# Kernel optimization log

Measured on AMD Instinct MI355X. Metric: run time of the kernel, lower is better.

The kernel has to match this reference:

```python
import jax, jax.numpy as jnp
import numpy as np

N_NODES = 100000
IN_DIM = 256
OUT_DIM = 128
N_EDGES = 3200000


def setup_inputs() -> dict:
    key = jax.random.key(0)
    k1, k2, k3, k4, k5, k6 = jax.random.split(key, 6)
    stdv = 1.0 / np.sqrt(OUT_DIM)
    return {
        "feature_map": jax.random.normal(k1, (N_NODES, IN_DIM), dtype=jnp.float32),
        "edge_src": jax.random.randint(k2, (N_EDGES,), 0, N_NODES, dtype=jnp.int32),
        "edge_dst": jax.random.randint(k3, (N_EDGES,), 0, N_NODES, dtype=jnp.int32),
        "edge_vals": jax.random.uniform(k4, (N_EDGES,), dtype=jnp.float32),
        "weights": jax.random.uniform(k5, (IN_DIM, OUT_DIM), dtype=jnp.float32, minval=-stdv, maxval=stdv),
        "b": jax.random.uniform(k6, (OUT_DIM,), dtype=jnp.float32, minval=-stdv, maxval=stdv),
    }


def reference(feature_map, edge_src, edge_dst, edge_vals, weights, b):
    # dense feature transform: [N, in] @ [in, out] -> [N, out]
    h = feature_map @ weights
    # sparse adjacency matmul A @ h via edge list:
    # out[dst] += A[dst, src] * h[src]
    msgs = edge_vals[:, None] * h[edge_src]  # [E, out]
    out = jax.ops.segment_sum(msgs, edge_dst, num_segments=N_NODES)
    # fused bias add epilogue
    return out + b
```

## Files before the change

### kernel.cpp

```cpp
#include <hip/hip_runtime.h>

#define N_NODES 100000
#define IN_DIM 256
#define OUT_DIM 128
#define N_EDGES 3200000

#define NB 3125
#define CAP 1280
#define PTILE 6400
#define PBLK 500
#define GBLK 782

typedef __attribute__((ext_vector_type(8))) short short8;
typedef __attribute__((ext_vector_type(4))) float float4v;

__device__ __forceinline__ unsigned short f2bf(float f) {
    union { float f; unsigned int u; } v; v.f = f;
    unsigned int r = v.u + 0x7FFF + ((v.u >> 16) & 1);
    return (unsigned short)(r >> 16);
}

__global__ __launch_bounds__(256) void setup_kernel(const float* __restrict__ W,
                                                    unsigned short* __restrict__ Wf,
                                                    int* __restrict__ cursor) {
    if (blockIdx.x < 16) {
        const int f = blockIdx.x * 256 + threadIdx.x;
        const int lane = f & 63;
        const int qc = f >> 6;
        const int q = qc >> 3, ct = qc & 7;
        const int n = ct * 16 + (lane & 15);
        const int k0 = q * 32 + (lane >> 4) * 8;
        unsigned int o[4];
#pragma unroll
        for (int jj = 0; jj < 4; ++jj) {
            const unsigned short lo = f2bf(W[(k0 + 2 * jj) * OUT_DIM + n]);
            const unsigned short hi = f2bf(W[(k0 + 2 * jj + 1) * OUT_DIM + n]);
            o[jj] = (unsigned)lo | ((unsigned)hi << 16);
        }
        ((uint4*)Wf)[f] = make_uint4(o[0], o[1], o[2], o[3]);
    } else {
        const int i = (blockIdx.x - 16) * 256 + threadIdx.x;
        if (i < NB) cursor[i] = 0;
    }
}

__global__ __launch_bounds__(512, 4) void fused_kernel(const float* __restrict__ X,
                                                       const unsigned short* __restrict__ Wf,
                                                       unsigned short* __restrict__ hb,
                                                       const int* __restrict__ src,
                                                       const int* __restrict__ dst,
                                                       const float* __restrict__ vals,
                                                       int* __restrict__ cursor,
                                                       int2* __restrict__ pairs) {
    __shared__ int smem[8192];
    const int tid = threadIdx.x;
    const int bx = blockIdx.x;
    const bool is_part = (bx < 1000) && ((bx & 1) == 0);

    if (is_part) {
        int* lhist = smem;
        int* lbase = smem + NB;
        const int pid = bx >> 1;
        const int base = pid * PTILE;

        for (int i = tid; i < NB; i += 512) lhist[i] = 0;
        __syncthreads();

        int   pk[13];
        int   sv[13];
        float vv[13];
#pragma unroll
        for (int k = 0; k < 13; ++k) {
            const int e = base + tid + k * 512;
            pk[k] = -1;
            if (tid + k * 512 < PTILE) {
                const int d = dst[e];
                const int b = d >> 5;
                const int r = atomicAdd(&lhist[b], 1);
                pk[k] = (b << 18) | (r << 5) | (d & 31);
                sv[k] = src[e];
                vv[k] = vals[e];
            }
        }
        __syncthreads();

        for (int i = tid; i < NB; i += 512) {
            const int c = lhist[i];
            if (c) lbase[i] = atomicAdd(&cursor[i], c);
        }
        __syncthreads();

#pragma unroll
        for (int k = 0; k < 13; ++k) {
            if (pk[k] >= 0) {
                const int b = pk[k] >> 18;
                const int r = (pk[k] >> 5) & 0x1FFF;
                const int pos = lbase[b] + r;
                if (pos < CAP)
                    pairs[(long)b * CAP + pos] =
                        make_int2(sv[k] | ((pk[k] & 31) << 20), __float_as_int(vv[k]));
            }
        }
    } else {
        const int gid = (bx < 1000) ? (bx >> 1) : (bx - 500);
        const int wid = tid >> 6;
        const int lane = tid & 63;
        const int m = lane & 15;
        const int quad = lane >> 4;
        const int row0 = gid * 128 + wid * 16;

        const int rl = min(row0 + m, N_NODES - 1);
        const float* xr = X + (long)rl * IN_DIM + quad * 8;
        short8 afrag[8];
#pragma unroll
        for (int q = 0; q < 8; ++q) {
            const float4 xa = *(const float4*)(xr + q * 32);
            const float4 xb = *(const float4*)(xr + q * 32 + 4);
            short8 f;
            f[0] = (short)f2bf(xa.x); f[1] = (short)f2bf(xa.y);
            f[2] = (short)f2bf(xa.z); f[3] = (short)f2bf(xa.w);
            f[4] = (short)f2bf(xb.x); f[5] = (short)f2bf(xb.y);
            f[6] = (short)f2bf(xb.z); f[7] = (short)f2bf(xb.w);
            afrag[q] = f;
        }

        unsigned short* stage = (unsigned short*)smem + wid * 2048;
        const short8* wfrag = (const short8*)Wf;
#pragma unroll 1
        for (int ct = 0; ct < 8; ++ct) {
            float4v acc = {0.f, 0.f, 0.f, 0.f};
#pragma unroll
            for (int q = 0; q < 8; ++q) {
                const short8 bfr = wfrag[(q * 8 + ct) * 64 + lane];
                acc = __builtin_amdgcn_mfma_f32_16x16x32_bf16(afrag[q], bfr, acc, 0, 0, 0);
            }
#pragma unroll
            for (int r = 0; r < 4; ++r)
                stage[(quad * 4 + r) * 128 + ct * 16 + m] = f2bf(acc[r]);
        }

#pragma unroll
        for (int j = 0; j < 4; ++j) {
            const uint4 vdata = *(const uint4*)(stage + j * 512 + lane * 8);
            const int row_r = row0 + j * 4 + quad;
            if (row_r < N_NODES)
                *(uint4*)(hb + (long)row_r * OUT_DIM + m * 8) = vdata;
        }
    }
}

__global__ __launch_bounds__(256) void gather_kernel(const int* __restrict__ cursor,
                                                     const int2* __restrict__ pairs,
                                                     const unsigned short* __restrict__ hb,
                                                     const float* __restrict__ bias,
                                                     float* __restrict__ out) {
    __shared__ int2 lp[CAP];
    __shared__ int rcnt[32];
    __shared__ int rbase[32];
    const int blk = blockIdx.x;
    const int tid = threadIdx.x;
    const int wid = tid >> 6;
    const int lane = tid & 63;

    const long beg = (long)blk * CAP;
    const int cnt = min(cursor[blk], CAP);

    if (tid < 32) rcnt[tid] = 0;
    __syncthreads();

    int2 sp[5];
    int  sr[5];
#pragma unroll
    for (int k = 0; k < 5; ++k) {
        const int i = tid + k * 256;
        sr[k] = -1;
        if (i < cnt) {
            const int2 p = pairs[beg + i];
            const int r = (p.x >> 20) & 31;
            const int rk = atomicAdd(&rcnt[r], 1);
            sp[k] = p;
            sr[k] = (r << 13) | rk;
        }
    }
    __syncthreads();

    if (wid == 0) {
        const int v = (lane < 32) ? rcnt[lane] : 0;
        int incl = v;
#pragma unroll
        for (int off = 1; off < 32; off <<= 1) {
            const int t = __shfl_up(incl, off);
            if (lane >= off) incl += t;
        }
        if (lane < 32) rbase[lane] = incl - v;
    }
    __syncthreads();

#pragma unroll
    for (int k = 0; k < 5; ++k) {
        if (sr[k] >= 0)
            lp[rbase[sr[k] >> 13] + (sr[k] & 0x1FFF)] = sp[k];
    }
    __syncthreads();

    const int half = lane >> 5;
    const int l5 = lane & 31;
    const int c4 = l5 * 4;
    const float4 bb = *(const float4*)(bias + c4);

#pragma unroll 1
    for (int rr = 0; rr < 8; ++rr) {
        const int r = wid * 8 + rr;
        const int node = blk * 32 + r;
        const int rb = rbase[r];
        const int re = rb + rcnt[r];

        float4 acc0 = {0.f, 0.f, 0.f, 0.f};
        float4 acc1 = {0.f, 0.f, 0.f, 0.f};

        for (int j = rb; j < re; j += 16) {
            int2 p[8];
#pragma unroll
            for (int t = 0; t < 8; ++t) {
                const int idx = j + 2 * t + half;
                int2 q = make_int2(0, 0);
                if (idx < re) q = lp[idx];
                p[t] = q;
            }
            uint2 u[8];
#pragma unroll
            for (int t = 0; t < 8; ++t)
                u[t] = *(const uint2*)(hb + (long)(p[t].x & 0xFFFFF) * OUT_DIM + c4);
#pragma unroll
            for (int t = 0; t < 8; ++t) {
                const float v = __int_as_float(p[t].y);
                const float f0 = __uint_as_float(u[t].x << 16);
                const float f1 = __uint_as_float(u[t].x & 0xFFFF0000u);
                const float f2 = __uint_as_float(u[t].y << 16);
                const float f3 = __uint_as_float(u[t].y & 0xFFFF0000u);
                if ((t & 1) == 0) {
                    acc0.x += v * f0; acc0.y += v * f1;
                    acc0.z += v * f2; acc0.w += v * f3;
                } else {
                    acc1.x += v * f0; acc1.y += v * f1;
                    acc1.z += v * f2; acc1.w += v * f3;
                }
            }
        }

        float4 s;
        s.x = acc0.x + acc1.x; s.y = acc0.y + acc1.y;
        s.z = acc0.z + acc1.z; s.w = acc0.w + acc1.w;
        s.x += __shfl_xor(s.x, 32);
        s.y += __shfl_xor(s.y, 32);
        s.z += __shfl_xor(s.z, 32);
        s.w += __shfl_xor(s.w, 32);
        if (half == 0) {
            float4 o = make_float4(bb.x + s.x, bb.y + s.y, bb.z + s.z, bb.w + s.w);
            *(float4*)(out + (long)node * OUT_DIM + c4) = o;
        }
    }
}

extern "C" void kernel_launch(void* const* d_in, const int* in_sizes, int n_in,
                              void* d_out, int out_size, void* d_ws, size_t ws_size,
                              hipStream_t stream) {
    const float* X     = (const float*)d_in[0];
    const int*   esrc  = (const int*)d_in[1];
    const int*   edst  = (const int*)d_in[2];
    const float* evals = (const float*)d_in[3];
    const float* W     = (const float*)d_in[4];
    const float* b     = (const float*)d_in[5];
    float* out = (float*)d_out;

    char* ws = (char*)d_ws;
    unsigned short* hb = (unsigned short*)(ws);
    int2* pairs        = (int2*)(ws + 25600000);
    int*  cursor       = (int*) (ws + 25600000 + 32000000);
    unsigned short* Wf = (unsigned short*)(ws + 57612512);

    setup_kernel<<<dim3(29), dim3(256), 0, stream>>>(W, Wf, cursor);
    fused_kernel<<<dim3(PBLK + GBLK), dim3(512), 0, stream>>>(X, Wf, hb,
                                                              esrc, edst, evals,
                                                              cursor, pairs);
    gather_kernel<<<dim3(NB), dim3(256), 0, stream>>>(cursor, pairs, hb, b, out);
}
```

Before: 364.2 us.

## Use larger partition tiles with two-pass histogram to cut global cursor atomics

Partition blocks now each handle 25600 edges instead of 6400, so there are 125 partition blocks instead of 500. They are interleaved every 7th block among the GEMM blocks. Because the larger tile cannot be held in registers, each partition block reads dst twice: one pass builds the local histogram and the next recomputes ranks with a cleared histogram. The intent is to cut global cursor atomics by about four times and spread partition work across the grid, at the cost of re-reading dst and more serial work per block.

```diff
diff --git a/kernel.cpp b/kernel.cpp
--- a/kernel.cpp
+++ b/kernel.cpp
@@ -7,9 +7,10 @@
 
 #define NB 3125
 #define CAP 1280
-#define PTILE 6400
-#define PBLK 500
+#define PTILE 25600
+#define PBLK 125
 #define GBLK 782
+#define NBLK (PBLK + GBLK)
 
 typedef __attribute__((ext_vector_type(8))) short short8;
 typedef __attribute__((ext_vector_type(4))) float float4v;
@@ -55,32 +56,21 @@
     __shared__ int smem[8192];
     const int tid = threadIdx.x;
     const int bx = blockIdx.x;
-    const bool is_part = (bx < 1000) && ((bx & 1) == 0);
+    const bool is_part = ((bx % 7) == 0) && (bx < 7 * PBLK);
 
     if (is_part) {
         int* lhist = smem;
         int* lbase = smem + NB;
-        const int pid = bx >> 1;
+        const int pid = bx / 7;
         const int base = pid * PTILE;
 
         for (int i = tid; i < NB; i += 512) lhist[i] = 0;
         __syncthreads();
 
-        int   pk[13];
-        int   sv[13];
-        float vv[13];
-#pragma unroll
-        for (int k = 0; k < 13; ++k) {
+#pragma unroll 2
+        for (int k = 0; k < 50; ++k) {
             const int e = base + tid + k * 512;
-            pk[k] = -1;
-            if (tid + k * 512 < PTILE) {
-                const int d = dst[e];
-                const int b = d >> 5;
-                const int r = atomicAdd(&lhist[b], 1);
-                pk[k] = (b << 18) | (r << 5) | (d & 31);
-                sv[k] = src[e];
-                vv[k] = vals[e];
-            }
+            atomicAdd(&lhist[dst[e] >> 5], 1);
         }
         __syncthreads();
 
@@ -89,20 +79,22 @@
             if (c) lbase[i] = atomicAdd(&cursor[i], c);
         }
         __syncthreads();
-
-#pragma unroll
-        for (int k = 0; k < 13; ++k) {
-            if (pk[k] >= 0) {
-                const int b = pk[k] >> 18;
-                const int r = (pk[k] >> 5) & 0x1FFF;
-                const int pos = lbase[b] + r;
-                if (pos < CAP)
-                    pairs[(long)b * CAP + pos] =
-                        make_int2(sv[k] | ((pk[k] & 31) << 20), __float_as_int(vv[k]));
-            }
+        for (int i = tid; i < NB; i += 512) lhist[i] = 0;
+        __syncthreads();
+
+#pragma unroll 2
+        for (int k = 0; k < 50; ++k) {
+            const int e = base + tid + k * 512;
+            const int d = dst[e];
+            const int b = d >> 5;
+            const int r = atomicAdd(&lhist[b], 1);
+            const int pos = lbase[b] + r;
+            if (pos < CAP)
+                pairs[(long)b * CAP + pos] =
+                    make_int2(src[e] | ((d & 31) << 20), __float_as_int(vals[e]));
         }
     } else {
-        const int gid = (bx < 1000) ? (bx >> 1) : (bx - 500);
+        const int gid = bx - min((bx + 6) / 7, PBLK);
         const int wid = tid >> 6;
         const int lane = tid & 63;
         const int m = lane & 15;
@@ -280,8 +272,8 @@
     unsigned short* Wf = (unsigned short*)(ws + 57612512);
 
     setup_kernel<<<dim3(29), dim3(256), 0, stream>>>(W, Wf, cursor);
-    fused_kernel<<<dim3(PBLK + GBLK), dim3(512), 0, stream>>>(X, Wf, hb,
-                                                              esrc, edst, evals,
-                                                              cursor, pairs);
+    fused_kernel<<<dim3(NBLK), dim3(512), 0, stream>>>(X, Wf, hb,
+                                                       esrc, edst, evals,
+                                                       cursor, pairs);
     gather_kernel<<<dim3(NB), dim3(256), 0, stream>>>(cursor, pairs, hb, b, out);
 }
```

New measurement: 413.0 us. +13.4%, slower.
